# Optimization experiments

Measured on AMD Instinct MI355X. Metric: run time of the kernel, lower is better.

Reference implementation:

```python
import jax, jax.numpy as jnp
import numpy as np

DELTA_V = 0.5
DELTA_D = 3.0
NUM_LANES = 4  # instance labels are 0 (background) .. NUM_LANES


def setup_inputs() -> dict:
    key = jax.random.key(0)
    k1, k2, k3 = jax.random.split(key, 3)
    B, E, H, W = 16, 4, 512, 1024
    pred = jax.random.normal(k1, (B, E, H, W), dtype=jnp.float32)
    binary_label = jax.random.randint(k2, (B, H, W), 0, 2).astype(jnp.float32)
    instance_label = jax.random.randint(k3, (B, H, W), 0, NUM_LANES + 1).astype(jnp.int32)
    return {"pred": pred, "binary_label": binary_label, "instance_label": instance_label}


def _forward(pred, binary_label, instance_label):
    B, E, H, W = pred.shape
    N = H * W
    C = NUM_LANES
    # masked embedding: zero out background per the binary mask
    pr = (binary_label[:, None, :, :] * pred).reshape(B, E, N)  # [B,E,N]
    pr = jnp.swapaxes(pr, 1, 2).reshape(B * N, E)               # [B*N,E]
    seg = (jnp.arange(B, dtype=jnp.int32)[:, None] * (C + 1)
           + instance_label.reshape(B, N)).reshape(-1)          # [B*N]
    nseg = B * (C + 1)
    sums = jax.ops.segment_sum(pr, seg, num_segments=nseg).reshape(B, C + 1, E)[:, 1:]      # [B,C,E]
    sumsq = jax.ops.segment_sum(pr * pr, seg, num_segments=nseg).reshape(B, C + 1, E)[:, 1:]
    counts = jax.ops.segment_sum(jnp.ones((B * N,), pred.dtype), seg,
                                 num_segments=nseg).reshape(B, C + 1)[:, 1:]                # [B,C]
    mu = sums / counts[..., None]                                # [B,C,E] cluster means
    # ||xi - mu||_F^2 over all masked pixels and channels of cluster c
    ssd = jnp.maximum((sumsq - counts[..., None] * mu * mu).sum(-1), 0.0)  # [B,C]
    nrm = jnp.sqrt(ssd)
    var = jnp.where(nrm > DELTA_V, (nrm - DELTA_V) ** 2, 0.0)
    L_var = var.mean()  # mean over all B*C cluster terms (matches sum/len)
    # pairwise center repulsion, ordered pairs i != j (double-counted as in original)
    diff = mu[:, :, None, :] - mu[:, None, :, :]                 # [B,C,C,E]
    d2 = (diff * diff).sum(-1)                                   # [B,C,C]
    eye = jnp.eye(C, dtype=bool)
    dist = jnp.sqrt(jnp.where(eye, 1.0, d2))
    dloss = jnp.where(eye, 0.0, jax.nn.relu(DELTA_D - dist) ** 2).sum((-1, -2))  # [B]
    L_dist = dloss.mean()
    return L_var + L_dist


def reference(pred, binary_label, instance_label):
    return _forward(pred, binary_label, instance_label)
```

## Files before the change

### kernel.cpp

```cpp
#include <hip/hip_runtime.h>

#define NB 16
#define NE 4
#define NC 4
#define NPIX (512 * 1024)

constexpr int THREADS = 256;
constexpr int BPB     = 128;
constexpr int UNITS   = NPIX / 4;
constexpr int ITERS   = UNITS / (BPB * THREADS);
#define WS_STRIDE 36

typedef float f32x4 __attribute__((ext_vector_type(4)));
typedef int   i32x4 __attribute__((ext_vector_type(4)));

__global__ __launch_bounds__(THREADS) void accum_kernel(
    const float* __restrict__ pred,
    const float* __restrict__ mask,
    const int*   __restrict__ inst,
    float* __restrict__ ws)
{
    const int b   = blockIdx.y;
    const int bx  = blockIdx.x;
    const int tid = threadIdx.x;

    float s[NC][NE] = {};
    float q[NC][NE] = {};
    float n[NC]     = {};

    const f32x4* pm  = reinterpret_cast<const f32x4*>(mask + (size_t)b * NPIX);
    const i32x4* pi  = reinterpret_cast<const i32x4*>(inst + (size_t)b * NPIX);
    const f32x4* pp0 = reinterpret_cast<const f32x4*>(pred + ((size_t)b * NE + 0) * NPIX);
    const f32x4* pp1 = reinterpret_cast<const f32x4*>(pred + ((size_t)b * NE + 1) * NPIX);
    const f32x4* pp2 = reinterpret_cast<const f32x4*>(pred + ((size_t)b * NE + 2) * NPIX);
    const f32x4* pp3 = reinterpret_cast<const f32x4*>(pred + ((size_t)b * NE + 3) * NPIX);

    #pragma unroll
    for (int k = 0; k < ITERS; ++k) {
        const int u = k * (BPB * THREADS) + bx * THREADS + tid;

        const f32x4 m4 = pm[u];
        const i32x4 i4 = pi[u];
        f32x4 p4[NE];
        p4[0] = pp0[u]; p4[1] = pp1[u]; p4[2] = pp2[u]; p4[3] = pp3[u];

        #pragma unroll
        for (int j = 0; j < 4; ++j) {
            const float mm  = m4[j];
            const int   lab = i4[j];
            float v[NE], sq[NE];
            #pragma unroll
            for (int e = 0; e < NE; ++e) {
                const float x = mm * p4[e][j];
                v[e]  = x;
                sq[e] = x * x;
            }
            #pragma unroll
            for (int c = 0; c < NC; ++c) {
                const float ind = (lab == c + 1) ? 1.0f : 0.0f;
                n[c] += ind;
                #pragma unroll
                for (int e = 0; e < NE; ++e) {
                    s[c][e] = fmaf(ind, v[e],  s[c][e]);
                    q[c][e] = fmaf(ind, sq[e], q[c][e]);
                }
            }
        }
    }

    #pragma unroll
    for (int c = 0; c < NC; ++c) {
        #pragma unroll
        for (int e = 0; e < NE; ++e) {
            s[c][e] += __shfl_xor(s[c][e], 1); s[c][e] += __shfl_xor(s[c][e], 2);
            q[c][e] += __shfl_xor(q[c][e], 1); q[c][e] += __shfl_xor(q[c][e], 2);
        }
        n[c] += __shfl_xor(n[c], 1); n[c] += __shfl_xor(n[c], 2);
    }

    __shared__ float red[64][WS_STRIDE];
    const int lane = tid & 63, wave = tid >> 6;
    if ((lane & 3) == 0) {
        float* dst = red[wave * 16 + (lane >> 2)];
        #pragma unroll
        for (int c = 0; c < NC; ++c) {
            #pragma unroll
            for (int e = 0; e < NE; ++e) {
                dst[c * 4 + e]      = s[c][e];
                dst[16 + c * 4 + e] = q[c][e];
            }
            dst[32 + c] = n[c];
        }
    }
    __syncthreads();

    if (tid < WS_STRIDE) {
        float tot = 0.0f;
        #pragma unroll
        for (int p2 = 0; p2 < 64; ++p2) tot += red[p2][tid];
        ws[((size_t)(b * BPB + bx)) * WS_STRIDE + tid] = tot;
    }
}

constexpr int FT = 640;
__global__ __launch_bounds__(FT) void finalize_kernel(
    const float* __restrict__ ws, float* __restrict__ out)
{
    __shared__ float fin[NB * WS_STRIDE];
    const int t = threadIdx.x;
    if (t < NB * WS_STRIDE) {
        const int b = t / WS_STRIDE, v = t % WS_STRIDE;
        float tot = 0.0f;
        #pragma unroll 8
        for (int blk = 0; blk < BPB; ++blk)
            tot += ws[((size_t)(b * BPB + blk)) * WS_STRIDE + v];
        fin[t] = tot;
    }
    __syncthreads();

    if (t < 64) {
        const int lane = t;
        const int b = lane >> 2;
        const int c = lane & 3;
        const float* wb = fin + b * WS_STRIDE;

        const float cnt = wb[32 + c];
        float mu[NE];
        float ssd = 0.0f;
        #pragma unroll
        for (int e = 0; e < NE; ++e) {
            const float sm = wb[c * 4 + e];
            const float qq = wb[16 + c * 4 + e];
            const float m  = sm / cnt;
            mu[e] = m;
            ssd += qq - cnt * m * m;
        }
        ssd = fmaxf(ssd, 0.0f);
        const float nrm = sqrtf(ssd);
        const float dv  = nrm - 0.5f;
        float var = (nrm > 0.5f) ? dv * dv : 0.0f;

        float dsum = 0.0f;
        const int qbase = lane & ~3;
        #pragma unroll
        for (int j = 0; j < NC; ++j) {
            float d2 = 0.0f;
            #pragma unroll
            for (int e = 0; e < NE; ++e) {
                const float mj = __shfl(mu[e], qbase + j);
                const float df = mu[e] - mj;
                d2 = fmaf(df, df, d2);
            }
            if (j != c) {
                const float dist = sqrtf(d2);
                const float r = fmaxf(3.0f - dist, 0.0f);
                dsum += r * r;
            }
        }

        #pragma unroll
        for (int off = 32; off; off >>= 1) {
            var  += __shfl_xor(var,  off);
            dsum += __shfl_xor(dsum, off);
        }
        if (lane == 0)
            out[0] = var / (float)(NB * NC) + dsum / (float)NB;
    }
}

extern "C" void kernel_launch(void* const* d_in, const int* in_sizes, int n_in,
                              void* d_out, int out_size, void* d_ws, size_t ws_size,
                              hipStream_t stream) {
    const float* pred = (const float*)d_in[0];
    const float* mask = (const float*)d_in[1];
    const int*   inst = (const int*)d_in[2];
    float* out = (float*)d_out;
    float* ws  = (float*)d_ws;

    dim3 grid(BPB, NB);
    accum_kernel<<<grid, THREADS, 0, stream>>>(pred, mask, inst, ws);
    finalize_kernel<<<1, FT, 0, stream>>>(ws, out);
}
```

Baseline: 240.3 us.

## Stream input tiles into LDS via global_load_lds with double buffering

Replaces direct per-thread global vector loads with asynchronous global-to-LDS copies (global_load_lds) into a double-buffered shared tile, so the next tile is staged while the current one is reduced. Block size goes to 512 threads and each block processes 16 tiles of 2048 pixels, which gives 16 blocks per batch instead of 128. The intent is to keep more memory traffic in flight and overlap loads with compute. The cost is a __syncthreads per tile, 96KB of LDS per block limiting occupancy, and far fewer blocks in the grid (256 total), which risks underfilling the GPU.

```diff
diff --git a/kernel.cpp b/kernel.cpp
--- a/kernel.cpp
+++ b/kernel.cpp
@@ -5,14 +5,39 @@
 #define NC 4
 #define NPIX (512 * 1024)
 
-constexpr int THREADS = 256;
-constexpr int BPB     = 128;
-constexpr int UNITS   = NPIX / 4;
-constexpr int ITERS   = UNITS / (BPB * THREADS);
+constexpr int THREADS         = 512;
+constexpr int TILE_PX         = 2048;
+constexpr int TILE_B          = TILE_PX * 4;
+constexpr int NSTREAM         = 6;
+constexpr int BUF_B           = NSTREAM * TILE_B;
+constexpr int TILES_PER_BLOCK = 16;
+constexpr int BPB             = (NPIX / TILE_PX) / TILES_PER_BLOCK;
 #define WS_STRIDE 36
 
 typedef float f32x4 __attribute__((ext_vector_type(4)));
 typedef int   i32x4 __attribute__((ext_vector_type(4)));
+
+__device__ __forceinline__ void stage_tile(
+    const char* __restrict__ predB, const char* __restrict__ maskB,
+    const char* __restrict__ instB, char* smem, int dbuf, int wave, int lane,
+    size_t px0)
+{
+    #pragma unroll
+    for (int i = 0; i < 6; ++i) {
+        const int idx = wave * 6 + i;
+        const int s   = idx >> 3;
+        const int run = idx & 7;
+        const char* g;
+        if (s < 4)       g = predB + (size_t)s * (NPIX * 4) + px0 * 4 + run * 1024;
+        else if (s == 4) g = maskB + px0 * 4 + run * 1024;
+        else             g = instB + px0 * 4 + run * 1024;
+        g += lane * 16;
+        char* l = smem + dbuf * BUF_B + s * TILE_B + run * 1024;
+        __builtin_amdgcn_global_load_lds(
+            (const __attribute__((address_space(1))) void*)g,
+            (__attribute__((address_space(3))) void*)l, 16, 0, 0);
+    }
+}
 
 __global__ __launch_bounds__(THREADS) void accum_kernel(
     const float* __restrict__ pred,
@@ -20,29 +45,42 @@
     const int*   __restrict__ inst,
     float* __restrict__ ws)
 {
-    const int b   = blockIdx.y;
-    const int bx  = blockIdx.x;
-    const int tid = threadIdx.x;
-
-    float s[NC][NE] = {};
-    float q[NC][NE] = {};
-    float n[NC]     = {};
-
-    const f32x4* pm  = reinterpret_cast<const f32x4*>(mask + (size_t)b * NPIX);
-    const i32x4* pi  = reinterpret_cast<const i32x4*>(inst + (size_t)b * NPIX);
-    const f32x4* pp0 = reinterpret_cast<const f32x4*>(pred + ((size_t)b * NE + 0) * NPIX);
-    const f32x4* pp1 = reinterpret_cast<const f32x4*>(pred + ((size_t)b * NE + 1) * NPIX);
-    const f32x4* pp2 = reinterpret_cast<const f32x4*>(pred + ((size_t)b * NE + 2) * NPIX);
-    const f32x4* pp3 = reinterpret_cast<const f32x4*>(pred + ((size_t)b * NE + 3) * NPIX);
-
-    #pragma unroll
-    for (int k = 0; k < ITERS; ++k) {
-        const int u = k * (BPB * THREADS) + bx * THREADS + tid;
-
-        const f32x4 m4 = pm[u];
-        const i32x4 i4 = pi[u];
+    __shared__ char smem[2 * BUF_B];
+
+    const int tid  = threadIdx.x;
+    const int wave = tid >> 6;
+    const int lane = tid & 63;
+    const int by   = blockIdx.y;
+    const int bx   = blockIdx.x;
+
+    const char* predB = (const char*)pred + (size_t)by * 4 * NPIX * 4;
+    const char* maskB = (const char*)mask + (size_t)by * NPIX * 4;
+    const char* instB = (const char*)inst + (size_t)by * NPIX * 4;
+    const size_t pxBase = (size_t)bx * (TILES_PER_BLOCK * TILE_PX);
+
+    float s_[NC][NE] = {};
+    float q_[NC][NE] = {};
+    float n_[NC]     = {};
+
+    stage_tile(predB, maskB, instB, smem, 0, wave, lane, pxBase);
+    __syncthreads();
+
+    #pragma unroll 1
+    for (int t = 0; t < TILES_PER_BLOCK; ++t) {
+        const int cur = t & 1, nxt = cur ^ 1;
+        if (t + 1 < TILES_PER_BLOCK)
+            stage_tile(predB, maskB, instB, smem, nxt, wave, lane,
+                       pxBase + (size_t)(t + 1) * TILE_PX);
+
+        const char* base = smem + cur * BUF_B;
+        const int   off  = tid * 16;
         f32x4 p4[NE];
-        p4[0] = pp0[u]; p4[1] = pp1[u]; p4[2] = pp2[u]; p4[3] = pp3[u];
+        p4[0] = *(const f32x4*)(base + 0 * TILE_B + off);
+        p4[1] = *(const f32x4*)(base + 1 * TILE_B + off);
+        p4[2] = *(const f32x4*)(base + 2 * TILE_B + off);
+        p4[3] = *(const f32x4*)(base + 3 * TILE_B + off);
+        const f32x4 m4 = *(const f32x4*)(base + 4 * TILE_B + off);
+        const i32x4 i4 = *(const i32x4*)(base + 5 * TILE_B + off);
 
         #pragma unroll
         for (int j = 0; j < 4; ++j) {
@@ -58,38 +96,38 @@
             #pragma unroll
             for (int c = 0; c < NC; ++c) {
                 const float ind = (lab == c + 1) ? 1.0f : 0.0f;
-                n[c] += ind;
+                n_[c] += ind;
                 #pragma unroll
                 for (int e = 0; e < NE; ++e) {
-                    s[c][e] = fmaf(ind, v[e],  s[c][e]);
-                    q[c][e] = fmaf(ind, sq[e], q[c][e]);
+                    s_[c][e] = fmaf(ind, v[e],  s_[c][e]);
+                    q_[c][e] = fmaf(ind, sq[e], q_[c][e]);
                 }
             }
         }
+        __syncthreads();
     }
 
     #pragma unroll
     for (int c = 0; c < NC; ++c) {
         #pragma unroll
         for (int e = 0; e < NE; ++e) {
-            s[c][e] += __shfl_xor(s[c][e], 1); s[c][e] += __shfl_xor(s[c][e], 2);
-            q[c][e] += __shfl_xor(q[c][e], 1); q[c][e] += __shfl_xor(q[c][e], 2);
-        }
-        n[c] += __shfl_xor(n[c], 1); n[c] += __shfl_xor(n[c], 2);
-    }
-
-    __shared__ float red[64][WS_STRIDE];
-    const int lane = tid & 63, wave = tid >> 6;
+            s_[c][e] += __shfl_xor(s_[c][e], 1); s_[c][e] += __shfl_xor(s_[c][e], 2);
+            q_[c][e] += __shfl_xor(q_[c][e], 1); q_[c][e] += __shfl_xor(q_[c][e], 2);
+        }
+        n_[c] += __shfl_xor(n_[c], 1); n_[c] += __shfl_xor(n_[c], 2);
+    }
+
+    float* redf = (float*)smem;
     if ((lane & 3) == 0) {
-        float* dst = red[wave * 16 + (lane >> 2)];
+        float* dst = redf + (wave * 16 + (lane >> 2)) * WS_STRIDE;
         #pragma unroll
         for (int c = 0; c < NC; ++c) {
             #pragma unroll
             for (int e = 0; e < NE; ++e) {
-                dst[c * 4 + e]      = s[c][e];
-                dst[16 + c * 4 + e] = q[c][e];
-            }
-            dst[32 + c] = n[c];
+                dst[c * 4 + e]      = s_[c][e];
+                dst[16 + c * 4 + e] = q_[c][e];
+            }
+            dst[32 + c] = n_[c];
         }
     }
     __syncthreads();
@@ -97,8 +135,8 @@
     if (tid < WS_STRIDE) {
         float tot = 0.0f;
         #pragma unroll
-        for (int p2 = 0; p2 < 64; ++p2) tot += red[p2][tid];
-        ws[((size_t)(b * BPB + bx)) * WS_STRIDE + tid] = tot;
+        for (int r = 0; r < 128; ++r) tot += redf[r * WS_STRIDE + tid];
+        ws[((size_t)(by * BPB + bx)) * WS_STRIDE + tid] = tot;
     }
 }
 
@@ -111,7 +149,7 @@
     if (t < NB * WS_STRIDE) {
         const int b = t / WS_STRIDE, v = t % WS_STRIDE;
         float tot = 0.0f;
-        #pragma unroll 8
+        #pragma unroll
         for (int blk = 0; blk < BPB; ++blk)
             tot += ws[((size_t)(b * BPB + blk)) * WS_STRIDE + v];
         fin[t] = tot;
```

Result: no change. 242.3 us (+0.8%).

## Split into label-packing pass and per-plane moment pass with byte keys

Applied to the files above, without the earlier changes.

Replaces the single fused accumulation kernel with three kernels. The first packs instance label and mask-nonzero flag into one byte per pixel and counts cluster sizes. The second reads each pred channel plane together with the byte keys and keeps only 8 accumulators per thread. The aim is to cut register pressure and per-pixel compute, at the cost of an extra launch, writing and re-reading the key buffer, a small 256-block grid, and treating the mask as binary rather than multiplying by it.

```diff
diff --git a/kernel.cpp b/kernel.cpp
--- a/kernel.cpp
+++ b/kernel.cpp
@@ -5,167 +5,189 @@
 #define NC 4
 #define NPIX (512 * 1024)
 
-constexpr int THREADS = 256;
-constexpr int BPB     = 128;
-constexpr int UNITS   = NPIX / 4;
-constexpr int ITERS   = UNITS / (BPB * THREADS);
-#define WS_STRIDE 36
-
 typedef float f32x4 __attribute__((ext_vector_type(4)));
 typedef int   i32x4 __attribute__((ext_vector_type(4)));
-
-__global__ __launch_bounds__(THREADS) void accum_kernel(
-    const float* __restrict__ pred,
-    const float* __restrict__ mask,
-    const int*   __restrict__ inst,
-    float* __restrict__ ws)
+typedef unsigned char u8;
+
+constexpr size_t KEYS_B = (size_t)NB * NPIX;
+
+constexpr int P1_THREADS = 512;
+constexpr int P1_CHUNKS  = 16;
+constexpr int P1_PXB     = NPIX / P1_CHUNKS;
+constexpr int P1_ITERS   = P1_PXB / (P1_THREADS * 4);
+
+constexpr int P2_THREADS = 512;
+constexpr int P2_CHUNKS  = 4;
+constexpr int P2_PXB     = NPIX / P2_CHUNKS;
+constexpr int P2_ITERS   = P2_PXB / (P2_THREADS * 4);
+
+__global__ __launch_bounds__(P1_THREADS) void key_kernel(
+    const float* __restrict__ mask, const int* __restrict__ inst,
+    u8* __restrict__ keys, float* __restrict__ npart)
 {
-    const int b   = blockIdx.y;
-    const int bx  = blockIdx.x;
-    const int tid = threadIdx.x;
-
-    float s[NC][NE] = {};
-    float q[NC][NE] = {};
-    float n[NC]     = {};
-
-    const f32x4* pm  = reinterpret_cast<const f32x4*>(mask + (size_t)b * NPIX);
-    const i32x4* pi  = reinterpret_cast<const i32x4*>(inst + (size_t)b * NPIX);
-    const f32x4* pp0 = reinterpret_cast<const f32x4*>(pred + ((size_t)b * NE + 0) * NPIX);
-    const f32x4* pp1 = reinterpret_cast<const f32x4*>(pred + ((size_t)b * NE + 1) * NPIX);
-    const f32x4* pp2 = reinterpret_cast<const f32x4*>(pred + ((size_t)b * NE + 2) * NPIX);
-    const f32x4* pp3 = reinterpret_cast<const f32x4*>(pred + ((size_t)b * NE + 3) * NPIX);
-
-    #pragma unroll
-    for (int k = 0; k < ITERS; ++k) {
-        const int u = k * (BPB * THREADS) + bx * THREADS + tid;
-
+    const int b = blockIdx.y, chunk = blockIdx.x, tid = threadIdx.x;
+    const size_t px0 = (size_t)chunk * P1_PXB;
+    const f32x4* pm = (const f32x4*)(mask + (size_t)b * NPIX + px0);
+    const i32x4* pi = (const i32x4*)(inst + (size_t)b * NPIX + px0);
+    unsigned int* ko = (unsigned int*)(keys + (size_t)b * NPIX + px0);
+
+    float n[NC] = {};
+
+    #pragma unroll 4
+    for (int it = 0; it < P1_ITERS; ++it) {
+        const int u = it * P1_THREADS + tid;
         const f32x4 m4 = pm[u];
         const i32x4 i4 = pi[u];
-        f32x4 p4[NE];
-        p4[0] = pp0[u]; p4[1] = pp1[u]; p4[2] = pp2[u]; p4[3] = pp3[u];
-
+        unsigned int packed = 0;
         #pragma unroll
         for (int j = 0; j < 4; ++j) {
+            const int   lab = i4[j];
             const float mm  = m4[j];
-            const int   lab = i4[j];
-            float v[NE], sq[NE];
+            const unsigned int k = (unsigned int)lab | (mm != 0.0f ? 8u : 0u);
+            packed |= k << (8 * j);
             #pragma unroll
-            for (int e = 0; e < NE; ++e) {
-                const float x = mm * p4[e][j];
-                v[e]  = x;
-                sq[e] = x * x;
-            }
+            for (int c = 0; c < NC; ++c)
+                n[c] += (lab == c + 1) ? 1.0f : 0.0f;
+        }
+        ko[u] = packed;
+    }
+
+    const int lane = tid & 63, wave = tid >> 6;
+    #pragma unroll
+    for (int c = 0; c < NC; ++c)
+        #pragma unroll
+        for (int off = 32; off; off >>= 1)
+            n[c] += __shfl_xor(n[c], off);
+
+    __shared__ float red[8][NC];
+    if (lane == 0) {
+        #pragma unroll
+        for (int c = 0; c < NC; ++c) red[wave][c] = n[c];
+    }
+    __syncthreads();
+    if (tid < NC) {
+        float t = 0.0f;
+        #pragma unroll
+        for (int w = 0; w < 8; ++w) t += red[w][tid];
+        npart[(b * P1_CHUNKS + chunk) * NC + tid] = t;
+    }
+}
+
+__global__ __launch_bounds__(P2_THREADS) void moment_kernel(
+    const float* __restrict__ pred, const u8* __restrict__ keys,
+    float* __restrict__ sqpart)
+{
+    const int chunk = blockIdx.x;
+    const int plane = blockIdx.y;
+    const int b     = plane >> 2;
+    const int tid   = threadIdx.x;
+    const size_t px0 = (size_t)chunk * P2_PXB;
+    const f32x4* pp = (const f32x4*)(pred + (size_t)plane * NPIX + px0);
+    const unsigned int* pk = (const unsigned int*)(keys + (size_t)b * NPIX + px0);
+
+    float s[NC] = {}, q[NC] = {};
+
+    #pragma unroll 4
+    for (int it = 0; it < P2_ITERS; ++it) {
+        const int u = it * P2_THREADS + tid;
+        const f32x4 p4 = pp[u];
+        const unsigned int k4 = pk[u];
+        #pragma unroll
+        for (int j = 0; j < 4; ++j) {
+            const float x  = p4[j];
+            const float x2 = x * x;
+            const int   k  = (int)((k4 >> (8 * j)) & 0xffu);
             #pragma unroll
             for (int c = 0; c < NC; ++c) {
-                const float ind = (lab == c + 1) ? 1.0f : 0.0f;
-                n[c] += ind;
-                #pragma unroll
-                for (int e = 0; e < NE; ++e) {
-                    s[c][e] = fmaf(ind, v[e],  s[c][e]);
-                    q[c][e] = fmaf(ind, sq[e], q[c][e]);
-                }
+                const float ind = (k == 9 + c) ? 1.0f : 0.0f;
+                s[c] = fmaf(ind, x,  s[c]);
+                q[c] = fmaf(ind, x2, q[c]);
             }
         }
     }
 
+    const int lane = tid & 63, wave = tid >> 6;
     #pragma unroll
     for (int c = 0; c < NC; ++c) {
         #pragma unroll
+        for (int off = 32; off; off >>= 1) {
+            s[c] += __shfl_xor(s[c], off);
+            q[c] += __shfl_xor(q[c], off);
+        }
+    }
+
+    __shared__ float red[8][8];
+    if (lane == 0) {
+        #pragma unroll
+        for (int c = 0; c < NC; ++c) { red[wave][c] = s[c]; red[wave][4 + c] = q[c]; }
+    }
+    __syncthreads();
+    if (tid < 8) {
+        float t = 0.0f;
+        #pragma unroll
+        for (int w = 0; w < 8; ++w) t += red[w][tid];
+        sqpart[((plane << 2) | chunk) * 8 + tid] = t;
+    }
+}
+
+__global__ __launch_bounds__(64) void finalize_kernel(
+    const float* __restrict__ npart, const float* __restrict__ sqpart,
+    float* __restrict__ out)
+{
+    const int lane = threadIdx.x;
+    const int b = lane >> 2;
+    const int c = lane & 3;
+
+    float cnt = 0.0f;
+    #pragma unroll
+    for (int ch = 0; ch < P1_CHUNKS; ++ch)
+        cnt += npart[(b * P1_CHUNKS + ch) * NC + c];
+
+    float mu[NE];
+    float ssd = 0.0f;
+    #pragma unroll
+    for (int e = 0; e < NE; ++e) {
+        const int plane = b * NE + e;
+        float se = 0.0f, qe = 0.0f;
+        #pragma unroll
+        for (int ch = 0; ch < P2_CHUNKS; ++ch) {
+            se += sqpart[((plane << 2) | ch) * 8 + c];
+            qe += sqpart[((plane << 2) | ch) * 8 + 4 + c];
+        }
+        const float m = se / cnt;
+        mu[e] = m;
+        ssd += qe - cnt * m * m;
+    }
+    ssd = fmaxf(ssd, 0.0f);
+    const float nrm = sqrtf(ssd);
+    const float dv  = nrm - 0.5f;
+    float var = (nrm > 0.5f) ? dv * dv : 0.0f;
+
+    float dsum = 0.0f;
+    const int qbase = lane & ~3;
+    #pragma unroll
+    for (int j = 0; j < NC; ++j) {
+        float d2 = 0.0f;
+        #pragma unroll
         for (int e = 0; e < NE; ++e) {
-            s[c][e] += __shfl_xor(s[c][e], 1); s[c][e] += __shfl_xor(s[c][e], 2);
-            q[c][e] += __shfl_xor(q[c][e], 1); q[c][e] += __shfl_xor(q[c][e], 2);
-        }
-        n[c] += __shfl_xor(n[c], 1); n[c] += __shfl_xor(n[c], 2);
-    }
-
-    __shared__ float red[64][WS_STRIDE];
-    const int lane = tid & 63, wave = tid >> 6;
-    if ((lane & 3) == 0) {
-        float* dst = red[wave * 16 + (lane >> 2)];
-        #pragma unroll
-        for (int c = 0; c < NC; ++c) {
-            #pragma unroll
-            for (int e = 0; e < NE; ++e) {
-                dst[c * 4 + e]      = s[c][e];
-                dst[16 + c * 4 + e] = q[c][e];
-            }
-            dst[32 + c] = n[c];
-        }
-    }
-    __syncthreads();
-
-    if (tid < WS_STRIDE) {
-        float tot = 0.0f;
-        #pragma unroll
-        for (int p2 = 0; p2 < 64; ++p2) tot += red[p2][tid];
-        ws[((size_t)(b * BPB + bx)) * WS_STRIDE + tid] = tot;
-    }
-}
-
-constexpr int FT = 640;
-__global__ __launch_bounds__(FT) void finalize_kernel(
-    const float* __restrict__ ws, float* __restrict__ out)
-{
-    __shared__ float fin[NB * WS_STRIDE];
-    const int t = threadIdx.x;
-    if (t < NB * WS_STRIDE) {
-        const int b = t / WS_STRIDE, v = t % WS_STRIDE;
-        float tot = 0.0f;
-        #pragma unroll 8
-        for (int blk = 0; blk < BPB; ++blk)
-            tot += ws[((size_t)(b * BPB + blk)) * WS_STRIDE + v];
-        fin[t] = tot;
-    }
-    __syncthreads();
-
-    if (t < 64) {
-        const int lane = t;
-        const int b = lane >> 2;
-        const int c = lane & 3;
-        const float* wb = fin + b * WS_STRIDE;
-
-        const float cnt = wb[32 + c];
-        float mu[NE];
-        float ssd = 0.0f;
-        #pragma unroll
-        for (int e = 0; e < NE; ++e) {
-            const float sm = wb[c * 4 + e];
-            const float qq = wb[16 + c * 4 + e];
-            const float m  = sm / cnt;
-            mu[e] = m;
-            ssd += qq - cnt * m * m;
-        }
-        ssd = fmaxf(ssd, 0.0f);
-        const float nrm = sqrtf(ssd);
-        const float dv  = nrm - 0.5f;
-        float var = (nrm > 0.5f) ? dv * dv : 0.0f;
-
-        float dsum = 0.0f;
-        const int qbase = lane & ~3;
-        #pragma unroll
-        for (int j = 0; j < NC; ++j) {
-            float d2 = 0.0f;
-            #pragma unroll
-            for (int e = 0; e < NE; ++e) {
-                const float mj = __shfl(mu[e], qbase + j);
-                const float df = mu[e] - mj;
-                d2 = fmaf(df, df, d2);
-            }
-            if (j != c) {
-                const float dist = sqrtf(d2);
-                const float r = fmaxf(3.0f - dist, 0.0f);
-                dsum += r * r;
-            }
-        }
-
-        #pragma unroll
-        for (int off = 32; off; off >>= 1) {
-            var  += __shfl_xor(var,  off);
-            dsum += __shfl_xor(dsum, off);
-        }
-        if (lane == 0)
-            out[0] = var / (float)(NB * NC) + dsum / (float)NB;
-    }
+            const float mj = __shfl(mu[e], qbase + j);
+            const float df = mu[e] - mj;
+            d2 = fmaf(df, df, d2);
+        }
+        if (j != c) {
+            const float dist = sqrtf(d2);
+            const float r = fmaxf(3.0f - dist, 0.0f);
+            dsum += r * r;
+        }
+    }
+
+    #pragma unroll
+    for (int off = 32; off; off >>= 1) {
+        var  += __shfl_xor(var,  off);
+        dsum += __shfl_xor(dsum, off);
+    }
+    if (lane == 0)
+        out[0] = var / (float)(NB * NC) + dsum / (float)NB;
 }
 
 extern "C" void kernel_launch(void* const* d_in, const int* in_sizes, int n_in,
@@ -175,9 +197,16 @@
     const float* mask = (const float*)d_in[1];
     const int*   inst = (const int*)d_in[2];
     float* out = (float*)d_out;
-    float* ws  = (float*)d_ws;
-
-    dim3 grid(BPB, NB);
-    accum_kernel<<<grid, THREADS, 0, stream>>>(pred, mask, inst, ws);
-    finalize_kernel<<<1, FT, 0, stream>>>(ws, out);
-}
+
+    u8*    keys   = (u8*)d_ws;
+    float* npart  = (float*)((char*)d_ws + KEYS_B);
+    float* sqpart = npart + 1024;
+
+    dim3 g1(P1_CHUNKS, NB);
+    key_kernel<<<g1, P1_THREADS, 0, stream>>>(mask, inst, keys, npart);
+
+    dim3 g2(P2_CHUNKS, NB * NE);
+    moment_kernel<<<g2, P2_THREADS, 0, stream>>>(pred, keys, sqpart);
+
+    finalize_kernel<<<1, 64, 0, stream>>>(npart, sqpart, out);
+}
```

Result: no change. 240.2 us (-0.0%).
